# Kernel optimization log

Hardware: AMD Instinct MI355X
Metric: run time of the kernel (lower is better)

Reference implementation:

```python
import jax, jax.numpy as jnp
import numpy as np

B, C, H, W = 64, 8, 256, 256
CQ = C // 8  # = 1, required for torch.matmul broadcasting in the original


def setup_inputs() -> dict:
    key = jax.random.key(0)
    ks = jax.random.split(key, 7)
    x = jax.random.normal(ks[0], (B, C, H, W), jnp.float32)
    # 1x1 conv weights stored as [out_ch, in_ch] (kernel dims squeezed)
    w1 = jax.random.normal(ks[1], (CQ, C), jnp.float32) * (1.0 / np.sqrt(C))
    b1 = jax.random.normal(ks[2], (CQ,), jnp.float32) * 0.01
    w2 = jax.random.normal(ks[3], (CQ, C), jnp.float32) * (1.0 / np.sqrt(C))
    b2 = jax.random.normal(ks[4], (CQ,), jnp.float32) * 0.01
    w3 = jax.random.normal(ks[5], (C, C), jnp.float32) * (1.0 / np.sqrt(C))
    b3 = jax.random.normal(ks[6], (C,), jnp.float32) * 0.01
    return {"x": x, "w1": w1, "b1": b1, "w2": w2, "b2": b2, "w3": w3, "b3": b3}


def reference(x, w1, b1, w2, b2, w3, b3):
    # 1x1 convs == channel contractions
    q = jnp.einsum('bchw,oc->bohw', x, w1) + b1[None, :, None, None]  # [B,1,H,W]
    k = jnp.einsum('bchw,oc->bohw', x, w2) + b2[None, :, None, None]  # [B,1,H,W]
    v = jnp.einsum('bchw,oc->bohw', x, w3) + b3[None, :, None, None]  # [B,C,H,W]
    # scores[b,i,j] = sum_w q[b,0,i,w] * k[b,0,j,w]   (q @ k^T over dims 2,3)
    scores = jnp.einsum('bhw,bgw->bhg', q[:, 0], k[:, 0])  # [B,H,H]
    attn = jax.nn.softmax(scores, axis=-1)
    # out[b,c,i,w] = sum_j attn[b,i,j] * v[b,c,j,w]  (broadcast over C)
    out = jnp.einsum('bhg,bcgw->bchw', attn, v)  # [B,C,H,W]
    return out
```

## Files before the change

### kernel.cpp

```cpp
#include <hip/hip_runtime.h>

typedef _Float16 h16;
typedef __attribute__((ext_vector_type(2))) _Float16 half2v;
typedef __attribute__((ext_vector_type(4))) _Float16 half4;
typedef __attribute__((ext_vector_type(8))) _Float16 half8;
typedef __attribute__((ext_vector_type(4))) float f32x4;

#define Cn 8
#define HWn 65536
#define CHWn 524288

__global__ __launch_bounds__(256) void prep_kernel(
    const float* __restrict__ x, const float* __restrict__ w1, const float* __restrict__ b1,
    const float* __restrict__ w2, const float* __restrict__ b2,
    const float* __restrict__ w3, const float* __restrict__ b3,
    h16* __restrict__ qh, h16* __restrict__ kh, h16* __restrict__ vt) {
  const int jt = blockIdx.x, wt = blockIdx.y, b = blockIdx.z;
  const int j0 = jt * 64, w0 = wt * 32;
  const int t = threadIdx.x;
  const int l = t & 15, jq = t >> 4;
  const int wb = w0 + 2 * l;
  const int jb = j0 + 4 * jq;
  __shared__ h16 lds[32 * 72];

  float qa[4][2], ka[4][2], va[8][4][2];
  const float bb1 = b1[0], bb2 = b2[0];
#pragma unroll
  for (int d = 0; d < 4; d++)
#pragma unroll
    for (int e = 0; e < 2; e++) { qa[d][e] = bb1; ka[d][e] = bb2; }
#pragma unroll
  for (int co = 0; co < 8; co++) {
    float bv = b3[co];
#pragma unroll
    for (int d = 0; d < 4; d++)
#pragma unroll
      for (int e = 0; e < 2; e++) va[co][d][e] = bv;
  }

  for (int ci = 0; ci < Cn; ci++) {
    const float* xp = x + ((size_t)(b * Cn + ci) << 16);
    const float w1c = w1[ci], w2c = w2[ci];
    float w3c[8];
#pragma unroll
    for (int co = 0; co < 8; co++) w3c[co] = w3[co * 8 + ci];
#pragma unroll
    for (int d = 0; d < 4; d++) {
      float2 xv = *(const float2*)&xp[(size_t)(jb + d) * 256 + wb];
      qa[d][0] = fmaf(xv.x, w1c, qa[d][0]); qa[d][1] = fmaf(xv.y, w1c, qa[d][1]);
      ka[d][0] = fmaf(xv.x, w2c, ka[d][0]); ka[d][1] = fmaf(xv.y, w2c, ka[d][1]);
#pragma unroll
      for (int co = 0; co < 8; co++) {
        va[co][d][0] = fmaf(xv.x, w3c[co], va[co][d][0]);
        va[co][d][1] = fmaf(xv.y, w3c[co], va[co][d][1]);
      }
    }
  }
#pragma unroll
  for (int d = 0; d < 4; d++) {
    half2v qv = {(h16)qa[d][0], (h16)qa[d][1]};
    half2v kv = {(h16)ka[d][0], (h16)ka[d][1]};
    size_t off = ((size_t)b << 16) + (size_t)(jb + d) * 256 + wb;
    *(half2v*)&qh[off] = qv;
    *(half2v*)&kh[off] = kv;
  }
  const int rrow = t >> 3;
  const int rch = t & 7;
  for (int co = 0; co < 8; co++) {
#pragma unroll
    for (int e = 0; e < 2; e++) {
      half4 hv = {(h16)va[co][0][e], (h16)va[co][1][e], (h16)va[co][2][e], (h16)va[co][3][e]};
      *(half4*)&lds[(2 * l + e) * 72 + 4 * jq] = hv;
    }
    __syncthreads();
    uint4 pk = *(const uint4*)&lds[rrow * 72 + 8 * rch];
    *(uint4*)&vt[((size_t)(b * Cn + co) * 256 + w0 + rrow) * 256 + j0 + 8 * rch] = pk;
    __syncthreads();
  }
}

__global__ __launch_bounds__(256) void scores_kernel(
    const h16* __restrict__ qh, const h16* __restrict__ kh, h16* __restrict__ p) {
  const int i0 = blockIdx.x * 16, b = blockIdx.y;
  const int t = threadIdx.x, wv = t >> 6, lane = t & 63;
  const int m = lane & 15, quad = lane >> 4;
  __shared__ float red[2][4][16];
  const h16* qrow = qh + ((size_t)b << 16) + (size_t)(i0 + m) * 256 + quad * 8;
  const h16* kbase = kh + ((size_t)b << 16) + (size_t)(wv * 64 + m) * 256 + quad * 8;
  f32x4 acc[4];
#pragma unroll
  for (int jt = 0; jt < 4; jt++) acc[jt] = {0.f, 0.f, 0.f, 0.f};
#pragma unroll
  for (int s = 0; s < 8; s++) {
    half8 Q = *(const half8*)(qrow + s * 32);
#pragma unroll
    for (int jt = 0; jt < 4; jt++) {
      half8 K = *(const half8*)(kbase + (size_t)jt * 4096 + s * 32);
      acc[jt] = __builtin_amdgcn_mfma_f32_16x16x32_f16(K, Q, acc[jt], 0, 0, 0);
    }
  }
  float mx = -3.4e38f;
#pragma unroll
  for (int jt = 0; jt < 4; jt++)
#pragma unroll
    for (int r = 0; r < 4; r++) mx = fmaxf(mx, acc[jt][r]);
  mx = fmaxf(mx, __shfl_xor(mx, 16, 64));
  mx = fmaxf(mx, __shfl_xor(mx, 32, 64));
  if (lane < 16) red[0][wv][lane] = mx;
  __syncthreads();
  float gmx = fmaxf(fmaxf(red[0][0][m], red[0][1][m]), fmaxf(red[0][2][m], red[0][3][m]));
  float sum = 0.f;
#pragma unroll
  for (int jt = 0; jt < 4; jt++)
#pragma unroll
    for (int r = 0; r < 4; r++) {
      float e = __expf(acc[jt][r] - gmx);
      acc[jt][r] = e;
      sum += e;
    }
  sum += __shfl_xor(sum, 16, 64);
  sum += __shfl_xor(sum, 32, 64);
  if (lane < 16) red[1][wv][lane] = sum;
  __syncthreads();
  const float inv = 1.f / (red[1][0][m] + red[1][1][m] + red[1][2][m] + red[1][3][m]);
  h16* pb = p + ((size_t)b << 16) + (size_t)(i0 + m) * 256;
#pragma unroll
  for (int jt = 0; jt < 4; jt++) {
    half4 pv = {(h16)(acc[jt][0] * inv), (h16)(acc[jt][1] * inv),
                (h16)(acc[jt][2] * inv), (h16)(acc[jt][3] * inv)};
    *(half4*)&pb[wv * 64 + jt * 16 + quad * 4] = pv;
  }
}

__global__ __launch_bounds__(256) void apply_kernel_mfma(
    const h16* __restrict__ p, const h16* __restrict__ vt, float* __restrict__ out) {
  const int bx = blockIdx.x, b = blockIdx.y;
  const int it = bx >> 4, nt = bx & 15;
  const int i0 = it * 128, n0 = nt * 128;
  const int t = threadIdx.x, wv = t >> 6, lane = t & 63;
  const int m = lane & 15, quad = lane >> 4;
  const int wy = wv >> 1, wx = wv & 1;
  __shared__ h16 As[128 * 40];
  __shared__ h16 Bs[128 * 40];
  const int srow = t >> 2, soff = (t & 3) * 8;
  const h16* gA = p + ((size_t)b << 16) + (size_t)(i0 + srow) * 256 + soff;
  const h16* gB = vt + (size_t)(b * 2048 + n0 + srow) * 256 + soff;
  uint4 ra0 = *(const uint4*)gA;
  uint4 ra1 = *(const uint4*)(gA + 64 * 256);
  uint4 rb0 = *(const uint4*)gB;
  uint4 rb1 = *(const uint4*)(gB + 64 * 256);
  f32x4 acc[4][4];
#pragma unroll
  for (int ai = 0; ai < 4; ai++)
#pragma unroll
    for (int bi = 0; bi < 4; bi++) acc[ai][bi] = {0.f, 0.f, 0.f, 0.f};
  const int lA = srow * 40 + soff;
  for (int kc = 0; kc < 8; kc++) {
    __syncthreads();
    *(uint4*)&As[lA] = ra0; *(uint4*)&As[lA + 64 * 40] = ra1;
    *(uint4*)&Bs[lA] = rb0; *(uint4*)&Bs[lA + 64 * 40] = rb1;
    __syncthreads();
    if (kc < 7) {
      const int ko = (kc + 1) * 32;
      ra0 = *(const uint4*)(gA + ko);
      ra1 = *(const uint4*)(gA + 64 * 256 + ko);
      rb0 = *(const uint4*)(gB + ko);
      rb1 = *(const uint4*)(gB + 64 * 256 + ko);
    }
    half8 af[4], bf[4];
#pragma unroll
    for (int ai = 0; ai < 4; ai++)
      af[ai] = *(const half8*)&As[(wy * 64 + ai * 16 + m) * 40 + quad * 8];
#pragma unroll
    for (int bi = 0; bi < 4; bi++)
      bf[bi] = *(const half8*)&Bs[(wx * 64 + bi * 16 + m) * 40 + quad * 8];
#pragma unroll
    for (int ai = 0; ai < 4; ai++)
#pragma unroll
      for (int bi = 0; bi < 4; bi++)
        acc[ai][bi] = __builtin_amdgcn_mfma_f32_16x16x32_f16(af[ai], bf[bi], acc[ai][bi], 0, 0, 0);
  }
  const int c = nt >> 1;
  const int wcol0 = (nt & 1) * 128 + wx * 64;
  float* ob = out + ((size_t)(b * Cn + c) << 16);
#pragma unroll
  for (int ai = 0; ai < 4; ai++) {
    const int ib = i0 + wy * 64 + ai * 16 + quad * 4;
#pragma unroll
    for (int r = 0; r < 4; r++)
#pragma unroll
      for (int bi = 0; bi < 4; bi++)
        ob[(size_t)(ib + r) * 256 + wcol0 + bi * 16 + m] = acc[ai][bi][r];
  }
}

__global__ __launch_bounds__(256) void qk_kernel(
    const float* __restrict__ x, const float* __restrict__ w1, const float* __restrict__ b1,
    const float* __restrict__ w2, const float* __restrict__ b2,
    float* __restrict__ q, float* __restrict__ k) {
  int n = blockIdx.x * 256 + threadIdx.x;
  int b = n >> 16;
  int pidx = n & 65535;
  const float* xb = x + (size_t)b * CHWn + pidx;
  float qa = b1[0], ka = b2[0];
#pragma unroll
  for (int c = 0; c < Cn; c++) {
    float xv = xb[c * HWn];
    qa = fmaf(xv, w1[c], qa);
    ka = fmaf(xv, w2[c], ka);
  }
  q[n] = qa;
  k[n] = ka;
}

__global__ __launch_bounds__(256) void scores_kernel_f32(
    const float* __restrict__ q, const float* __restrict__ k, float* __restrict__ sc) {
  const int jt = blockIdx.x, it = blockIdx.y, b = blockIdx.z;
  const int i0 = it * 128, j0 = jt * 128;
  const int t = threadIdx.x;
  const int tx = t & 15, ty = t >> 4;
  __shared__ __align__(16) float qt[32 * 132];
  __shared__ __align__(16) float kt[32 * 132];
  float acc[2][2][4][4];
#pragma unroll
  for (int a = 0; a < 2; a++)
#pragma unroll
    for (int bb = 0; bb < 2; bb++)
#pragma unroll
      for (int il = 0; il < 4; il++)
#pragma unroll
        for (int jl = 0; jl < 4; jl++) acc[a][bb][il][jl] = 0.f;
  const float* qb = q + (size_t)b * HWn;
  const float* kb = k + (size_t)b * HWn;
  for (int kc = 0; kc < 8; kc++) {
    const int w0 = kc * 32;
    __syncthreads();
#pragma unroll
    for (int e = 0; e < 16; e++) {
      int idx = t + 256 * e;
      int r = idx >> 5, c = idx & 31;
      qt[c * 132 + r] = qb[(i0 + r) * 256 + w0 + c];
      kt[c * 132 + r] = kb[(j0 + r) * 256 + w0 + c];
    }
    __syncthreads();
#pragma unroll 4
    for (int w = 0; w < 32; w++) {
      const float4 a0 = *(const float4*)&qt[w * 132 + ty * 4];
      const float4 a1 = *(const float4*)&qt[w * 132 + 64 + ty * 4];
      const float4 b0 = *(const float4*)&kt[w * 132 + tx * 4];
      const float4 b1 = *(const float4*)&kt[w * 132 + 64 + tx * 4];
      const float av[2][4] = {{a0.x, a0.y, a0.z, a0.w}, {a1.x, a1.y, a1.z, a1.w}};
      const float bv[2][4] = {{b0.x, b0.y, b0.z, b0.w}, {b1.x, b1.y, b1.z, b1.w}};
#pragma unroll
      for (int ih = 0; ih < 2; ih++)
#pragma unroll
        for (int jh = 0; jh < 2; jh++)
#pragma unroll
          for (int il = 0; il < 4; il++)
#pragma unroll
            for (int jl = 0; jl < 4; jl++)
              acc[ih][jh][il][jl] = fmaf(av[ih][il], bv[jh][jl], acc[ih][jh][il][jl]);
    }
  }
  float* scb = sc + (size_t)b * HWn;
#pragma unroll
  for (int ih = 0; ih < 2; ih++)
#pragma unroll
    for (int il = 0; il < 4; il++) {
      int i = i0 + ih * 64 + ty * 4 + il;
#pragma unroll
      for (int jh = 0; jh < 2; jh++) {
        float4 st = make_float4(acc[ih][jh][il][0], acc[ih][jh][il][1],
                                acc[ih][jh][il][2], acc[ih][jh][il][3]);
        *(float4*)&scb[i * 256 + j0 + jh * 64 + tx * 4] = st;
      }
    }
}

__global__ __launch_bounds__(256) void softmax_kernel(float* __restrict__ at) {
  int wave = (blockIdx.x * 256 + threadIdx.x) >> 6;
  int lane = threadIdx.x & 63;
  float* row = at + (size_t)wave * 256;
  float v[4];
  float mm = -3.4e38f;
#pragma unroll
  for (int u = 0; u < 4; u++) {
    v[u] = row[lane + 64 * u];
    mm = fmaxf(mm, v[u]);
  }
#pragma unroll
  for (int o = 1; o < 64; o <<= 1) mm = fmaxf(mm, __shfl_xor(mm, o, 64));
  float s = 0.f;
#pragma unroll
  for (int u = 0; u < 4; u++) {
    v[u] = __expf(v[u] - mm);
    s += v[u];
  }
#pragma unroll
  for (int o = 1; o < 64; o <<= 1) s += __shfl_xor(s, o, 64);
  float inv = 1.0f / s;
#pragma unroll
  for (int u = 0; u < 4; u++) row[lane + 64 * u] = v[u] * inv;
}

__global__ __launch_bounds__(256, 2) void apply_kernel(
    const float* __restrict__ x, const float* __restrict__ at,
    const float* __restrict__ w3, const float* __restrict__ b3, float* __restrict__ out) {
  const int it = blockIdx.x, b = blockIdx.y;
  const int i0 = it * 16;
  const int t = threadIdx.x;
  __shared__ __align__(16) float pt[16 * 256];
  const float* atb = at + (size_t)b * HWn + i0 * 256;
#pragma unroll
  for (int e = 0; e < 4; e++)
    *(float4*)&pt[t * 4 + 1024 * e] = *(const float4*)&atb[t * 4 + 1024 * e];
  __syncthreads();
  float acc[8][16];
#pragma unroll
  for (int c = 0; c < 8; c++)
#pragma unroll
    for (int ii = 0; ii < 16; ii++) acc[c][ii] = 0.f;
  const float* xb = x + (size_t)b * CHWn + t;
  for (int j0 = 0; j0 < 256; j0 += 2) {
    float p2[16][2];
#pragma unroll
    for (int ii = 0; ii < 16; ii++) {
      float2 pp = *(const float2*)&pt[ii * 256 + j0];
      p2[ii][0] = pp.x;
      p2[ii][1] = pp.y;
    }
#pragma unroll
    for (int ju = 0; ju < 2; ju++) {
      float xv[8];
#pragma unroll
      for (int c = 0; c < 8; c++) xv[c] = xb[c * HWn + (j0 + ju) * 256];
#pragma unroll
      for (int c = 0; c < 8; c++)
#pragma unroll
        for (int ii = 0; ii < 16; ii++)
          acc[c][ii] = fmaf(xv[c], p2[ii][ju], acc[c][ii]);
    }
  }
#pragma unroll
  for (int co = 0; co < 8; co++) {
    float wr[8];
#pragma unroll
    for (int ci = 0; ci < 8; ci++) wr[ci] = w3[co * 8 + ci];
    float bb = b3[co];
#pragma unroll
    for (int ii = 0; ii < 16; ii++) {
      float o = bb;
#pragma unroll
      for (int ci = 0; ci < 8; ci++) o = fmaf(wr[ci], acc[ci][ii], o);
      out[(size_t)b * CHWn + co * HWn + (i0 + ii) * 256 + t] = o;
    }
  }
}

extern "C" void kernel_launch(void* const* d_in, const int* in_sizes, int n_in,
                              void* d_out, int out_size, void* d_ws, size_t ws_size,
                              hipStream_t stream) {
  const float* x  = (const float*)d_in[0];
  const float* w1 = (const float*)d_in[1];
  const float* b1 = (const float*)d_in[2];
  const float* w2 = (const float*)d_in[3];
  const float* b2 = (const float*)d_in[4];
  const float* w3 = (const float*)d_in[5];
  const float* b3 = (const float*)d_in[6];
  float* out = (float*)d_out;

  if (ws_size >= (size_t)92274688) {
    char* wsb = (char*)d_ws;
    h16* vt = (h16*)wsb;
    h16* qh = (h16*)(wsb + 67108864);
    h16* kh = (h16*)(wsb + 75497472);
    h16* p  = (h16*)(wsb + 83886080);
    prep_kernel<<<dim3(4, 8, 64), dim3(256), 0, stream>>>(x, w1, b1, w2, b2, w3, b3, qh, kh, vt);
    scores_kernel<<<dim3(16, 64), dim3(256), 0, stream>>>(qh, kh, p);
    apply_kernel_mfma<<<dim3(32, 64), dim3(256), 0, stream>>>(p, vt, out);
  } else {
    float* wsf = (float*)d_ws;
    float* q  = wsf;
    float* k  = wsf + 4194304;
    float* at = wsf + 8388608;
    qk_kernel<<<dim3(16384), dim3(256), 0, stream>>>(x, w1, b1, w2, b2, q, k);
    scores_kernel_f32<<<dim3(2, 2, 64), dim3(256), 0, stream>>>(q, k, at);
    softmax_kernel<<<dim3(4096), dim3(256), 0, stream>>>(at);
    apply_kernel<<<dim3(16, 64), dim3(256), 0, stream>>>(x, at, w3, b3, out);
  }
}
```

Baseline: 309.7 us.

## Restructure prep kernel into 32x32 tiles with upfront float4 loads and single-sync transpose

Each thread of the prep kernel now issues all eight channel loads as float4s up front, covering 4 contiguous w values, in place of per-channel float2 loads in a loop. The block tile shrinks from 64x32 to 32x32, so twice as many blocks launch. All eight v channels are staged in padded shared memory with one barrier, instead of the two barriers per channel used before. The aim is more memory-level parallelism and fewer syncs in this bandwidth-bound stage, at the cost of more shared memory and strided 2-byte LDS reads during the transpose.

```diff
diff --git a/kernel.cpp b/kernel.cpp
--- a/kernel.cpp
+++ b/kernel.cpp
@@ -10,72 +10,80 @@
 #define HWn 65536
 #define CHWn 524288
 
+#define PADW 42
 __global__ __launch_bounds__(256) void prep_kernel(
     const float* __restrict__ x, const float* __restrict__ w1, const float* __restrict__ b1,
     const float* __restrict__ w2, const float* __restrict__ b2,
     const float* __restrict__ w3, const float* __restrict__ b3,
     h16* __restrict__ qh, h16* __restrict__ kh, h16* __restrict__ vt) {
-  const int jt = blockIdx.x, wt = blockIdx.y, b = blockIdx.z;
-  const int j0 = jt * 64, w0 = wt * 32;
+  const int wt = blockIdx.x, jt = blockIdx.y, b = blockIdx.z;
+  const int j0 = jt * 32, w0 = wt * 32;
   const int t = threadIdx.x;
-  const int l = t & 15, jq = t >> 4;
-  const int wb = w0 + 2 * l;
-  const int jb = j0 + 4 * jq;
-  __shared__ h16 lds[32 * 72];
-
-  float qa[4][2], ka[4][2], va[8][4][2];
+  const int jl = t >> 3, wq = t & 7;
+  __shared__ h16 sv[8 * 32 * PADW];
+
+  float4 xv[8];
+  const float* xb = x + ((size_t)b << 19) + (size_t)(j0 + jl) * 256 + w0 + wq * 4;
+#pragma unroll
+  for (int ci = 0; ci < 8; ci++)
+    xv[ci] = *(const float4*)(xb + ((size_t)ci << 16));
+
+  float qa[4], ka[4], va[8][4];
   const float bb1 = b1[0], bb2 = b2[0];
 #pragma unroll
-  for (int d = 0; d < 4; d++)
-#pragma unroll
-    for (int e = 0; e < 2; e++) { qa[d][e] = bb1; ka[d][e] = bb2; }
+  for (int e = 0; e < 4; e++) { qa[e] = bb1; ka[e] = bb2; }
 #pragma unroll
   for (int co = 0; co < 8; co++) {
-    float bv = b3[co];
-#pragma unroll
-    for (int d = 0; d < 4; d++)
-#pragma unroll
-      for (int e = 0; e < 2; e++) va[co][d][e] = bv;
-  }
-
-  for (int ci = 0; ci < Cn; ci++) {
-    const float* xp = x + ((size_t)(b * Cn + ci) << 16);
+    const float bv = b3[co];
+#pragma unroll
+    for (int e = 0; e < 4; e++) va[co][e] = bv;
+  }
+#pragma unroll
+  for (int ci = 0; ci < 8; ci++) {
+    const float xe[4] = {xv[ci].x, xv[ci].y, xv[ci].z, xv[ci].w};
     const float w1c = w1[ci], w2c = w2[ci];
-    float w3c[8];
-#pragma unroll
-    for (int co = 0; co < 8; co++) w3c[co] = w3[co * 8 + ci];
-#pragma unroll
-    for (int d = 0; d < 4; d++) {
-      float2 xv = *(const float2*)&xp[(size_t)(jb + d) * 256 + wb];
-      qa[d][0] = fmaf(xv.x, w1c, qa[d][0]); qa[d][1] = fmaf(xv.y, w1c, qa[d][1]);
-      ka[d][0] = fmaf(xv.x, w2c, ka[d][0]); ka[d][1] = fmaf(xv.y, w2c, ka[d][1]);
-#pragma unroll
-      for (int co = 0; co < 8; co++) {
-        va[co][d][0] = fmaf(xv.x, w3c[co], va[co][d][0]);
-        va[co][d][1] = fmaf(xv.y, w3c[co], va[co][d][1]);
-      }
-    }
-  }
-#pragma unroll
-  for (int d = 0; d < 4; d++) {
-    half2v qv = {(h16)qa[d][0], (h16)qa[d][1]};
-    half2v kv = {(h16)ka[d][0], (h16)ka[d][1]};
-    size_t off = ((size_t)b << 16) + (size_t)(jb + d) * 256 + wb;
-    *(half2v*)&qh[off] = qv;
-    *(half2v*)&kh[off] = kv;
-  }
-  const int rrow = t >> 3;
-  const int rch = t & 7;
+#pragma unroll
+    for (int e = 0; e < 4; e++) {
+      qa[e] = fmaf(xe[e], w1c, qa[e]);
+      ka[e] = fmaf(xe[e], w2c, ka[e]);
+    }
+#pragma unroll
+    for (int co = 0; co < 8; co++) {
+      const float w3c = w3[co * 8 + ci];
+#pragma unroll
+      for (int e = 0; e < 4; e++) va[co][e] = fmaf(xe[e], w3c, va[co][e]);
+    }
+  }
+
+  {
+    half4 qv = {(h16)qa[0], (h16)qa[1], (h16)qa[2], (h16)qa[3]};
+    half4 kv = {(h16)ka[0], (h16)ka[1], (h16)ka[2], (h16)ka[3]};
+    size_t off = ((size_t)b << 16) + (size_t)(j0 + jl) * 256 + w0 + wq * 4;
+    *(half4*)&qh[off] = qv;
+    *(half4*)&kh[off] = kv;
+  }
+
+#pragma unroll
   for (int co = 0; co < 8; co++) {
-#pragma unroll
-    for (int e = 0; e < 2; e++) {
-      half4 hv = {(h16)va[co][0][e], (h16)va[co][1][e], (h16)va[co][2][e], (h16)va[co][3][e]};
-      *(half4*)&lds[(2 * l + e) * 72 + 4 * jq] = hv;
-    }
-    __syncthreads();
-    uint4 pk = *(const uint4*)&lds[rrow * 72 + 8 * rch];
-    *(uint4*)&vt[((size_t)(b * Cn + co) * 256 + w0 + rrow) * 256 + j0 + 8 * rch] = pk;
-    __syncthreads();
+    half2v v01 = {(h16)va[co][0], (h16)va[co][1]};
+    half2v v23 = {(h16)va[co][2], (h16)va[co][3]};
+    h16* p = &sv[co * 32 * PADW + jl * PADW + wq * 4];
+    *(half2v*)p = v01;
+    *(half2v*)(p + 2) = v23;
+  }
+  __syncthreads();
+
+#pragma unroll
+  for (int cc = 0; cc < 4; cc++) {
+    const int cid = t + 256 * cc;
+    const int co = cid >> 7;
+    const int w = (cid >> 2) & 31;
+    const int jc = cid & 3;
+    const h16* rp = &sv[co * 32 * PADW + (jc * 8) * PADW + w];
+    half8 pk;
+#pragma unroll
+    for (int e = 0; e < 8; e++) pk[e] = rp[e * PADW];
+    *(half8*)&vt[((size_t)(b * Cn + co) * 256 + w0 + w) * 256 + j0 + jc * 8] = pk;
   }
 }
 
@@ -375,7 +383,7 @@
     h16* qh = (h16*)(wsb + 67108864);
     h16* kh = (h16*)(wsb + 75497472);
     h16* p  = (h16*)(wsb + 83886080);
-    prep_kernel<<<dim3(4, 8, 64), dim3(256), 0, stream>>>(x, w1, b1, w2, b2, w3, b3, qh, kh, vt);
+    prep_kernel<<<dim3(8, 8, 64), dim3(256), 0, stream>>>(x, w1, b1, w2, b2, w3, b3, qh, kh, vt);
     scores_kernel<<<dim3(16, 64), dim3(256), 0, stream>>>(qh, kh, p);
     apply_kernel_mfma<<<dim3(32, 64), dim3(256), 0, stream>>>(p, vt, out);
   } else {
```

New measurement: 308.3 us. Within noise of the previous version (-0.4%).
